# Optimization experiments

Measured on AMD Instinct MI355X. Metric: run time of the kernel, lower is better.

Reference implementation:

```python
import jax, jax.numpy as jnp
import numpy as np

D = 64        # d_model = hidden_units
DK = 64       # d_k (softmax scale)
EPS = 1e-5    # torch LayerNorm default eps


def setup_inputs() -> dict:
    key = jax.random.key(0)
    ks = jax.random.split(key, 5)
    x = jax.random.normal(ks[0], (4, 4, 2048, D), dtype=jnp.float32)
    # nn.Linear weight shape is [out, in]; y = x @ W.T
    W_Q = jax.random.normal(ks[1], (D, D), dtype=jnp.float32) * 0.05
    W_K = jax.random.normal(ks[2], (D, D), dtype=jnp.float32) * 0.05
    W_V = jax.random.normal(ks[3], (D, D), dtype=jnp.float32) * 0.05
    W_fc = jax.random.normal(ks[4], (D, D), dtype=jnp.float32) * 0.05
    return {"x": x, "W_Q": W_Q, "W_K": W_K, "W_V": W_V, "W_fc": W_fc}


def reference(x, W_Q, W_K, W_V, W_fc):
    # x: [B, X, S, D]
    Q = jnp.einsum('bxsd,ed->bxse', x, W_Q)
    K = jnp.einsum('bxsd,ed->bxse', x, W_K)
    V = jnp.einsum('bxsd,ed->bxse', x, W_V)
    scale = 1.0 / np.sqrt(DK).astype(np.float32)
    scores = jnp.einsum('bxqe,bxke->bxqk', Q, K) * scale  # [B,X,S,S]
    attn = jax.nn.softmax(scores, axis=-1)                # mask is dead code in original
    context = jnp.einsum('bxqk,bxke->bxqe', attn, V)
    out = jnp.einsum('bxse,fe->bxsf', context, W_fc) + x  # fc + residual
    # LayerNorm with default (unit gamma, zero beta)
    mean = jnp.mean(out, axis=-1, keepdims=True)
    var = jnp.var(out, axis=-1, keepdims=True)
    return (out - mean) / jnp.sqrt(var + EPS)
```

## Files before the change

kernel.cpp:

```cpp
#include <hip/hip_runtime.h>
#include <math.h>


#define HEADS 16
#define SEQ   2048
#define DIM   64
#define NT    32

typedef short short8 __attribute__((ext_vector_type(8)));
typedef short short4v __attribute__((ext_vector_type(4)));
typedef float f32x4  __attribute__((ext_vector_type(4)));

__device__ __align__(16) short g_Qh [(size_t)HEADS * SEQ * DIM];
__device__ __align__(16) short g_Qm [(size_t)HEADS * SEQ * DIM];
__device__ __align__(16) short g_Ql [(size_t)HEADS * SEQ * DIM];
__device__ __align__(16) short g_Kh [(size_t)HEADS * SEQ * DIM];
__device__ __align__(16) short g_Km [(size_t)HEADS * SEQ * DIM];
__device__ __align__(16) short g_Kl [(size_t)HEADS * SEQ * DIM];
__device__ __align__(16) short g_VTh[(size_t)HEADS * DIM * SEQ];
__device__ __align__(16) short g_VTm[(size_t)HEADS * DIM * SEQ];
__device__ __align__(16) short g_VTl[(size_t)HEADS * DIM * SEQ];

static __device__ __forceinline__ short f2bf(float f) {
  union { float f; unsigned u; } cv; cv.f = f;
  unsigned u = cv.u;
  unsigned r = (u + 0x7fffu + ((u >> 16) & 1u)) >> 16;
  return (short)r;
}
static __device__ __forceinline__ float bf2f(short s) {
  union { unsigned u; float f; } cv; cv.u = ((unsigned)(unsigned short)s) << 16;
  return cv.f;
}
static __device__ __forceinline__ void split2(float v, short* h, short* l) {
  short hh = f2bf(v);
  *h = hh;
  *l = f2bf(v - bf2f(hh));
}
static __device__ __forceinline__ short2 split2v(float v) {
  short hh = f2bf(v);
  short ll = f2bf(v - bf2f(hh));
  return make_short2(hh, ll);
}
static __device__ __forceinline__ void split3(float v, short* h, short* m, short* l) {
  short hh = f2bf(v);
  float r  = v - bf2f(hh);
  short mm = f2bf(r);
  *h = hh; *m = mm;
  *l = f2bf(r - bf2f(mm));
}
static __device__ __forceinline__ void split3_bits(float v, short* h, short* m, short* l) {
  union { float f; unsigned u; } a; a.f = v;
  unsigned hu = a.u & 0xFFFF0000u;
  union { unsigned u; float f; } hf; hf.u = hu;
  float r = v - hf.f;
  union { float f; unsigned u; } b; b.f = r;
  unsigned mu = b.u & 0xFFFF0000u;
  union { unsigned u; float f; } mf; mf.u = mu;
  union { float f; unsigned u; } c2; c2.f = r - mf.f;
  *h = (short)(hu >> 16); *m = (short)(mu >> 16); *l = (short)(c2.u >> 16);
}

__global__ __launch_bounds__(256) void qkv_valu(
    const float* __restrict__ x,  const float* __restrict__ WQ,
    const float* __restrict__ WK, const float* __restrict__ WV)
{
  __shared__ float XB [64][68];
  __shared__ float WTQ[64][68];
  __shared__ float WTK[64][68];
  __shared__ float WTV[64][68];
  const int t    = threadIdx.x;
  const int head = blockIdx.x >> 5;
  const int s0   = (blockIdx.x & 31) * 64;
  const float* xp = x + ((size_t)head * SEQ + s0) * DIM;

  for (int i = t; i < 1024; i += 256) {
    int row = i >> 4, c4 = (i & 15) << 2;
    *(float4*)&XB[row][c4] = *(const float4*)(xp + row * 64 + c4);
    float4 a = *(const float4*)(WQ + row * 64 + c4);
    WTQ[c4][row] = a.x; WTQ[c4+1][row] = a.y; WTQ[c4+2][row] = a.z; WTQ[c4+3][row] = a.w;
    float4 b = *(const float4*)(WK + row * 64 + c4);
    WTK[c4][row] = b.x; WTK[c4+1][row] = b.y; WTK[c4+2][row] = b.z; WTK[c4+3][row] = b.w;
    float4 d = *(const float4*)(WV + row * 64 + c4);
    WTV[c4][row] = d.x; WTV[c4+1][row] = d.y; WTV[c4+2][row] = d.z; WTV[c4+3][row] = d.w;
  }
  __syncthreads();

  const int jj = t >> 2;
  const int eg = (t & 3) * 16;
  float aq[16], ak[16], av[16];
#pragma unroll
  for (int c = 0; c < 16; ++c) { aq[c] = 0.f; ak[c] = 0.f; av[c] = 0.f; }
  for (int d = 0; d < 64; ++d) {
    float xv = XB[jj][d];
#pragma unroll
    for (int c4 = 0; c4 < 16; c4 += 4) {
      float4 wq = *(const float4*)&WTQ[d][eg + c4];
      aq[c4]   += xv * wq.x; aq[c4+1] += xv * wq.y; aq[c4+2] += xv * wq.z; aq[c4+3] += xv * wq.w;
      float4 wk = *(const float4*)&WTK[d][eg + c4];
      ak[c4]   += xv * wk.x; ak[c4+1] += xv * wk.y; ak[c4+2] += xv * wk.z; ak[c4+3] += xv * wk.w;
      float4 wv = *(const float4*)&WTV[d][eg + c4];
      av[c4]   += xv * wv.x; av[c4+1] += xv * wv.y; av[c4+2] += xv * wv.z; av[c4+3] += xv * wv.w;
    }
  }
  const size_t rowi  = ((size_t)head * SEQ + s0 + jj) * DIM + eg;
  const size_t vbase = (size_t)head * DIM * SEQ + s0 + jj;
  short qh_[16], qm_[16], ql_[16], kh_[16], km_[16], kl_[16];
#pragma unroll
  for (int c = 0; c < 16; ++c) {
    split3(aq[c] * 0.125f, &qh_[c], &qm_[c], &ql_[c]);
    split3(ak[c],          &kh_[c], &km_[c], &kl_[c]);
    size_t vb = vbase + (size_t)(eg + c) * SEQ;
    split3(av[c], &g_VTh[vb], &g_VTm[vb], &g_VTl[vb]);
  }
#pragma unroll
  for (int half = 0; half < 2; ++half) {
    *(short8*)(g_Qh + rowi + half*8) = *(const short8*)&qh_[half*8];
    *(short8*)(g_Qm + rowi + half*8) = *(const short8*)&qm_[half*8];
    *(short8*)(g_Ql + rowi + half*8) = *(const short8*)&ql_[half*8];
    *(short8*)(g_Kh + rowi + half*8) = *(const short8*)&kh_[half*8];
    *(short8*)(g_Km + rowi + half*8) = *(const short8*)&km_[half*8];
    *(short8*)(g_Kl + rowi + half*8) = *(const short8*)&kl_[half*8];
  }
}

__global__ __launch_bounds__(512) void attn_mfma(
    const float* __restrict__ x, const float* __restrict__ Wfc, float* __restrict__ out)
{
  __shared__ short Kth[64][72],  Ktm[64][72],  Ktl[64][72];
  __shared__ short Vth[64][72],  Vtm[64][72],  Vtl[64][72];
  __shared__ short Pth[128][72], Ptm[128][72], Ptl[128][72];
  const int t    = threadIdx.x;
  const int w    = t >> 6, lane = t & 63;
  const int r16  = lane & 15, g = lane >> 4;
  const int wq   = w & 3;
  const int wk   = (w >> 2) & 1;
  const int head = blockIdx.x >> 4;
  const int q0   = (blockIdx.x & 15) * 128;
  const short* Kph = g_Kh  + (size_t)head * SEQ * DIM;
  const short* Kpm = g_Km  + (size_t)head * SEQ * DIM;
  const short* Kpl = g_Kl  + (size_t)head * SEQ * DIM;
  const short* Vph = g_VTh + (size_t)head * DIM * SEQ;
  const short* Vpm = g_VTm + (size_t)head * DIM * SEQ;
  const short* Vpl = g_VTl + (size_t)head * DIM * SEQ;
  const int srow = t >> 3, scol = (t & 7) * 8;

  short8 qfh[2][2], qfm[2][2], qfl[2][2];
#pragma unroll
  for (int qs = 0; qs < 2; ++qs) {
    const size_t qrow = ((size_t)head * SEQ + q0 + wq*32 + qs*16 + r16) * DIM;
#pragma unroll
    for (int dh = 0; dh < 2; ++dh) {
      qfh[qs][dh] = *(const short8*)(g_Qh + qrow + dh*32 + g*8);
      qfm[qs][dh] = *(const short8*)(g_Qm + qrow + dh*32 + g*8);
      qfl[qs][dh] = *(const short8*)(g_Ql + qrow + dh*32 + g*8);
    }
  }

  short8 rkh, rkm, rkl, rvh, rvm, rvl;
  {
    size_t ko = (size_t)srow * 64 + scol;
    rkh = *(const short8*)(Kph + ko);
    rkm = *(const short8*)(Kpm + ko);
    rkl = *(const short8*)(Kpl + ko);
    size_t vo = (size_t)srow * SEQ + scol;
    rvh = *(const short8*)(Vph + vo);
    rvm = *(const short8*)(Vpm + vo);
    rvl = *(const short8*)(Vpl + vo);
  }

  f32x4 o[2][4];
  float lacc[2];
#pragma unroll
  for (int qs = 0; qs < 2; ++qs) {
    lacc[qs] = 0.f;
#pragma unroll
    for (int ne = 0; ne < 4; ++ne) o[qs][ne] = (f32x4){0.f,0.f,0.f,0.f};
  }

  for (int kt = 0; kt < NT; ++kt) {
    __syncthreads();
    *(short8*)&Kth[srow][scol] = rkh;
    *(short8*)&Ktm[srow][scol] = rkm;
    *(short8*)&Ktl[srow][scol] = rkl;
    *(short8*)&Vth[srow][scol] = rvh;
    *(short8*)&Vtm[srow][scol] = rvm;
    *(short8*)&Vtl[srow][scol] = rvl;
    __syncthreads();
    if (kt + 1 < NT) {
      size_t ko = (size_t)((kt+1)*64 + srow) * 64 + scol;
      rkh = *(const short8*)(Kph + ko);
      rkm = *(const short8*)(Kpm + ko);
      rkl = *(const short8*)(Kpl + ko);
      size_t vo = (size_t)srow * SEQ + (kt+1)*64 + scol;
      rvh = *(const short8*)(Vph + vo);
      rvm = *(const short8*)(Vpm + vo);
      rvl = *(const short8*)(Vpl + vo);
    }

    f32x4 sa[2][2];
#pragma unroll
    for (int qs = 0; qs < 2; ++qs)
#pragma unroll
      for (int n = 0; n < 2; ++n) sa[qs][n] = (f32x4){0.f,0.f,0.f,0.f};
#pragma unroll
    for (int n = 0; n < 2; ++n) {
#pragma unroll
      for (int dh = 0; dh < 2; ++dh) {
        short8 akh = *(const short8*)&Kth[wk*32 + n*16 + r16][dh*32 + g*8];
        short8 akm = *(const short8*)&Ktm[wk*32 + n*16 + r16][dh*32 + g*8];
        short8 akl = *(const short8*)&Ktl[wk*32 + n*16 + r16][dh*32 + g*8];
#pragma unroll
        for (int qs = 0; qs < 2; ++qs) {
          sa[qs][n] = __builtin_amdgcn_mfma_f32_16x16x32_bf16(akh, qfh[qs][dh], sa[qs][n], 0, 0, 0);
          sa[qs][n] = __builtin_amdgcn_mfma_f32_16x16x32_bf16(akh, qfm[qs][dh], sa[qs][n], 0, 0, 0);
          sa[qs][n] = __builtin_amdgcn_mfma_f32_16x16x32_bf16(akm, qfh[qs][dh], sa[qs][n], 0, 0, 0);
          sa[qs][n] = __builtin_amdgcn_mfma_f32_16x16x32_bf16(akh, qfl[qs][dh], sa[qs][n], 0, 0, 0);
          sa[qs][n] = __builtin_amdgcn_mfma_f32_16x16x32_bf16(akm, qfm[qs][dh], sa[qs][n], 0, 0, 0);
          sa[qs][n] = __builtin_amdgcn_mfma_f32_16x16x32_bf16(akl, qfh[qs][dh], sa[qs][n], 0, 0, 0);
        }
      }
    }
#pragma unroll
    for (int qs = 0; qs < 2; ++qs) {
#pragma unroll
      for (int n = 0; n < 2; ++n) {
        short hh[4], mm[4], ll[4];
#pragma unroll
        for (int r = 0; r < 4; ++r) {
          float p = __expf(sa[qs][n][r]);
          lacc[qs] += p;
          split3_bits(p, &hh[r], &mm[r], &ll[r]);
        }
        const int prow = wq*32 + qs*16 + r16;
        const int pcol = wk*32 + n*16 + g*4;
        short4v vh4; vh4[0]=hh[0]; vh4[1]=hh[1]; vh4[2]=hh[2]; vh4[3]=hh[3];
        short4v vm4; vm4[0]=mm[0]; vm4[1]=mm[1]; vm4[2]=mm[2]; vm4[3]=mm[3];
        short4v vl4; vl4[0]=ll[0]; vl4[1]=ll[1]; vl4[2]=ll[2]; vl4[3]=ll[3];
        *(short4v*)&Pth[prow][pcol] = vh4;
        *(short4v*)&Ptm[prow][pcol] = vm4;
        *(short4v*)&Ptl[prow][pcol] = vl4;
      }
    }
    asm volatile("s_waitcnt lgkmcnt(0)" ::: "memory");
    __builtin_amdgcn_sched_barrier(0);
    short8 aph[2], apm[2], apl[2];
#pragma unroll
    for (int qs = 0; qs < 2; ++qs) {
      aph[qs] = *(const short8*)&Pth[wq*32 + qs*16 + r16][wk*32 + g*8];
      apm[qs] = *(const short8*)&Ptm[wq*32 + qs*16 + r16][wk*32 + g*8];
      apl[qs] = *(const short8*)&Ptl[wq*32 + qs*16 + r16][wk*32 + g*8];
    }
#pragma unroll
    for (int ne = 0; ne < 4; ++ne) {
      short8 bvh = *(const short8*)&Vth[ne*16 + r16][wk*32 + g*8];
      short8 bvm = *(const short8*)&Vtm[ne*16 + r16][wk*32 + g*8];
      short8 bvl = *(const short8*)&Vtl[ne*16 + r16][wk*32 + g*8];
#pragma unroll
      for (int qs = 0; qs < 2; ++qs) {
        o[qs][ne] = __builtin_amdgcn_mfma_f32_16x16x32_bf16(aph[qs], bvh, o[qs][ne], 0, 0, 0);
        o[qs][ne] = __builtin_amdgcn_mfma_f32_16x16x32_bf16(aph[qs], bvm, o[qs][ne], 0, 0, 0);
        o[qs][ne] = __builtin_amdgcn_mfma_f32_16x16x32_bf16(apm[qs], bvh, o[qs][ne], 0, 0, 0);
        o[qs][ne] = __builtin_amdgcn_mfma_f32_16x16x32_bf16(aph[qs], bvl, o[qs][ne], 0, 0, 0);
        o[qs][ne] = __builtin_amdgcn_mfma_f32_16x16x32_bf16(apm[qs], bvm, o[qs][ne], 0, 0, 0);
        o[qs][ne] = __builtin_amdgcn_mfma_f32_16x16x32_bf16(apl[qs], bvh, o[qs][ne], 0, 0, 0);
      }
    }
  }

  float lr[2];
#pragma unroll
  for (int qs = 0; qs < 2; ++qs) {
    float s = lacc[qs];
    s += __shfl_xor(s, 16);
    s += __shfl_xor(s, 32);
    lr[qs] = s;
  }

  __syncthreads();
#pragma unroll
  for (int qs = 0; qs < 2; ++qs)
    split3(lr[qs], &Pth[wq*32 + qs*16 + r16][64 + wk],
                   &Ptm[wq*32 + qs*16 + r16][64 + wk],
                   &Ptl[wq*32 + qs*16 + r16][64 + wk]);
  if (wk == 1) {
#pragma unroll
    for (int qs = 0; qs < 2; ++qs)
#pragma unroll
      for (int ne = 0; ne < 4; ++ne)
#pragma unroll
        for (int r = 0; r < 4; ++r) {
          int row = wq*32 + qs*16 + g*4 + r, col = ne*16 + r16;
          split3(o[qs][ne][r], &Pth[row][col], &Ptm[row][col], &Ptl[row][col]);
        }
  }
  __syncthreads();
  float lt[2][4];
  if (wk == 0) {
#pragma unroll
    for (int qs = 0; qs < 2; ++qs) {
#pragma unroll
      for (int ne = 0; ne < 4; ++ne)
#pragma unroll
        for (int r = 0; r < 4; ++r) {
          int row = wq*32 + qs*16 + g*4 + r, col = ne*16 + r16;
          o[qs][ne][r] += bf2f(Pth[row][col]) + bf2f(Ptm[row][col]) + bf2f(Ptl[row][col]);
        }
#pragma unroll
      for (int r = 0; r < 4; ++r) {
        int row = wq*32 + qs*16 + g*4 + r;
        lt[qs][r] = bf2f(Pth[row][64]) + bf2f(Ptm[row][64]) + bf2f(Ptl[row][64])
                  + bf2f(Pth[row][65]) + bf2f(Ptm[row][65]) + bf2f(Ptl[row][65]);
      }
    }
  }
  asm volatile("s_waitcnt lgkmcnt(0)" ::: "memory");
  __builtin_amdgcn_sched_barrier(0);

  if (wk == 0) {
#pragma unroll
    for (int qs = 0; qs < 2; ++qs)
#pragma unroll
      for (int ne = 0; ne < 4; ++ne)
#pragma unroll
        for (int r = 0; r < 4; ++r) {
          int row = wq*32 + qs*16 + g*4 + r, col = ne*16 + r16;
          split2(o[qs][ne][r] / lt[qs][r], &Pth[row][col], &Ptl[row][col]);
        }
    asm volatile("s_waitcnt lgkmcnt(0)" ::: "memory");
    __builtin_amdgcn_sched_barrier(0);
#pragma unroll
    for (int qs = 0; qs < 2; ++qs) {
      short8 cah[2], cal[2];
#pragma unroll
      for (int ks = 0; ks < 2; ++ks) {
        cah[ks] = *(const short8*)&Pth[wq*32 + qs*16 + r16][ks*32 + g*8];
        cal[ks] = *(const short8*)&Ptl[wq*32 + qs*16 + r16][ks*32 + g*8];
      }
      float res[4][4];
      float sum[4], sq[4];
#pragma unroll
      for (int r = 0; r < 4; ++r) { sum[r] = 0.f; sq[r] = 0.f; }
#pragma unroll
      for (int n = 0; n < 4; ++n) {
        const float* wrow = Wfc + (n*16 + r16) * 64;
        f32x4 fca = (f32x4){0.f,0.f,0.f,0.f};
#pragma unroll
        for (int ks = 0; ks < 2; ++ks) {
          float4 w0 = *(const float4*)(wrow + ks*32 + g*8);
          float4 w1 = *(const float4*)(wrow + ks*32 + g*8 + 4);
          short8 bh, bl;
          short2 s0 = split2v(w0.x); bh[0] = s0.x; bl[0] = s0.y;
          short2 s1 = split2v(w0.y); bh[1] = s1.x; bl[1] = s1.y;
          short2 s2 = split2v(w0.z); bh[2] = s2.x; bl[2] = s2.y;
          short2 s3 = split2v(w0.w); bh[3] = s3.x; bl[3] = s3.y;
          short2 s4 = split2v(w1.x); bh[4] = s4.x; bl[4] = s4.y;
          short2 s5 = split2v(w1.y); bh[5] = s5.x; bl[5] = s5.y;
          short2 s6 = split2v(w1.z); bh[6] = s6.x; bl[6] = s6.y;
          short2 s7 = split2v(w1.w); bh[7] = s7.x; bl[7] = s7.y;
          fca = __builtin_amdgcn_mfma_f32_16x16x32_bf16(cah[ks], bh, fca, 0, 0, 0);
          fca = __builtin_amdgcn_mfma_f32_16x16x32_bf16(cah[ks], bl, fca, 0, 0, 0);
          fca = __builtin_amdgcn_mfma_f32_16x16x32_bf16(cal[ks], bh, fca, 0, 0, 0);
        }
#pragma unroll
        for (int r = 0; r < 4; ++r) {
          float v = fca[r] +
            x[((size_t)head * SEQ + q0 + wq*32 + qs*16 + g*4 + r) * 64 + n*16 + r16];
          res[n][r] = v;
          sum[r] += v;
          sq[r]  += v * v;
        }
      }
#pragma unroll
      for (int r = 0; r < 4; ++r) {
        float s = sum[r], q2 = sq[r];
        s += __shfl_xor(s, 1);  q2 += __shfl_xor(q2, 1);
        s += __shfl_xor(s, 2);  q2 += __shfl_xor(q2, 2);
        s += __shfl_xor(s, 4);  q2 += __shfl_xor(q2, 4);
        s += __shfl_xor(s, 8);  q2 += __shfl_xor(q2, 8);
        float mean = s * (1.f/64.f);
        float var  = q2 * (1.f/64.f) - mean * mean;
        float rstd = rsqrtf(var + 1e-5f);
        float* op = out + ((size_t)head * SEQ + q0 + wq*32 + qs*16 + g*4 + r) * 64 + r16;
#pragma unroll
        for (int n = 0; n < 4; ++n)
          op[n*16] = (res[n][r] - mean) * rstd;
      }
    }
  }
}

extern "C" void kernel_launch(void* const* d_in, const int* in_sizes, int n_in,
                              void* d_out, int out_size, void* d_ws, size_t ws_size,
                              hipStream_t stream) {
  const float* x  = (const float*)d_in[0];
  const float* WQ = (const float*)d_in[1];
  const float* WK = (const float*)d_in[2];
  const float* WV = (const float*)d_in[3];
  const float* Wf = (const float*)d_in[4];
  float* out = (float*)d_out;
  (void)d_ws; (void)ws_size; (void)in_sizes; (void)n_in; (void)out_size;
  qkv_valu<<<dim3(512), dim3(256), 0, stream>>>(x, WQ, WK, WV);
  attn_mfma<<<dim3(256), dim3(512), 0, stream>>>(x, Wf, out);
}
```

Before: 123.6 us.

## Load K/V MFMA operands directly from global memory, dropping LDS staging

Result: slower. 267.1 us (+116.1%).

```diff
diff --git a/kernel.cpp b/kernel.cpp
--- a/kernel.cpp
+++ b/kernel.cpp
@@ -123,11 +123,9 @@
   }
 }
 
-__global__ __launch_bounds__(512) void attn_mfma(
+__global__ __launch_bounds__(512, 4) void attn_mfma(
     const float* __restrict__ x, const float* __restrict__ Wfc, float* __restrict__ out)
 {
-  __shared__ short Kth[64][72],  Ktm[64][72],  Ktl[64][72];
-  __shared__ short Vth[64][72],  Vtm[64][72],  Vtl[64][72];
   __shared__ short Pth[128][72], Ptm[128][72], Ptl[128][72];
   const int t    = threadIdx.x;
   const int w    = t >> 6, lane = t & 63;
@@ -142,7 +140,6 @@
   const short* Vph = g_VTh + (size_t)head * DIM * SEQ;
   const short* Vpm = g_VTm + (size_t)head * DIM * SEQ;
   const short* Vpl = g_VTl + (size_t)head * DIM * SEQ;
-  const int srow = t >> 3, scol = (t & 7) * 8;
 
   short8 qfh[2][2], qfm[2][2], qfl[2][2];
 #pragma unroll
@@ -156,18 +153,6 @@
     }
   }
 
-  short8 rkh, rkm, rkl, rvh, rvm, rvl;
-  {
-    size_t ko = (size_t)srow * 64 + scol;
-    rkh = *(const short8*)(Kph + ko);
-    rkm = *(const short8*)(Kpm + ko);
-    rkl = *(const short8*)(Kpl + ko);
-    size_t vo = (size_t)srow * SEQ + scol;
-    rvh = *(const short8*)(Vph + vo);
-    rvm = *(const short8*)(Vpm + vo);
-    rvl = *(const short8*)(Vpl + vo);
-  }
-
   f32x4 o[2][4];
   float lacc[2];
 #pragma unroll
@@ -178,25 +163,6 @@
   }
 
   for (int kt = 0; kt < NT; ++kt) {
-    __syncthreads();
-    *(short8*)&Kth[srow][scol] = rkh;
-    *(short8*)&Ktm[srow][scol] = rkm;
-    *(short8*)&Ktl[srow][scol] = rkl;
-    *(short8*)&Vth[srow][scol] = rvh;
-    *(short8*)&Vtm[srow][scol] = rvm;
-    *(short8*)&Vtl[srow][scol] = rvl;
-    __syncthreads();
-    if (kt + 1 < NT) {
-      size_t ko = (size_t)((kt+1)*64 + srow) * 64 + scol;
-      rkh = *(const short8*)(Kph + ko);
-      rkm = *(const short8*)(Kpm + ko);
-      rkl = *(const short8*)(Kpl + ko);
-      size_t vo = (size_t)srow * SEQ + (kt+1)*64 + scol;
-      rvh = *(const short8*)(Vph + vo);
-      rvm = *(const short8*)(Vpm + vo);
-      rvl = *(const short8*)(Vpl + vo);
-    }
-
     f32x4 sa[2][2];
 #pragma unroll
     for (int qs = 0; qs < 2; ++qs)
@@ -206,9 +172,10 @@
     for (int n = 0; n < 2; ++n) {
 #pragma unroll
       for (int dh = 0; dh < 2; ++dh) {
-        short8 akh = *(const short8*)&Kth[wk*32 + n*16 + r16][dh*32 + g*8];
-        short8 akm = *(const short8*)&Ktm[wk*32 + n*16 + r16][dh*32 + g*8];
-        short8 akl = *(const short8*)&Ktl[wk*32 + n*16 + r16][dh*32 + g*8];
+        const size_t ko = (size_t)(kt*64 + wk*32 + n*16 + r16) * 64 + dh*32 + g*8;
+        short8 akh = *(const short8*)(Kph + ko);
+        short8 akm = *(const short8*)(Kpm + ko);
+        short8 akl = *(const short8*)(Kpl + ko);
 #pragma unroll
         for (int qs = 0; qs < 2; ++qs) {
           sa[qs][n] = __builtin_amdgcn_mfma_f32_16x16x32_bf16(akh, qfh[qs][dh], sa[qs][n], 0, 0, 0);
@@ -252,9 +219,10 @@
     }
 #pragma unroll
     for (int ne = 0; ne < 4; ++ne) {
-      short8 bvh = *(const short8*)&Vth[ne*16 + r16][wk*32 + g*8];
-      short8 bvm = *(const short8*)&Vtm[ne*16 + r16][wk*32 + g*8];
-      short8 bvl = *(const short8*)&Vtl[ne*16 + r16][wk*32 + g*8];
+      const size_t vo = (size_t)(ne*16 + r16) * SEQ + kt*64 + wk*32 + g*8;
+      short8 bvh = *(const short8*)(Vph + vo);
+      short8 bvm = *(const short8*)(Vpm + vo);
+      short8 bvl = *(const short8*)(Vpl + vo);
 #pragma unroll
       for (int qs = 0; qs < 2; ++qs) {
         o[qs][ne] = __builtin_amdgcn_mfma_f32_16x16x32_bf16(aph[qs], bvh, o[qs][ne], 0, 0, 0);
```
